# Kernel optimization log

Measured on AMD Instinct MI355X. Metric: run time of the kernel, lower is better.

The kernel has to match this reference:

```python
import jax, jax.numpy as jnp
import numpy as np

EMBED_DIM = 2048
HEAD_DIM = 128
BLOCK = 2048
BATCH = 8


def setup_inputs() -> dict:
    key = jax.random.key(0)
    kx, kq, kk, kv = jax.random.split(key, 4)
    x = jax.random.normal(kx, (BATCH, BLOCK, EMBED_DIM), dtype=jnp.float32)
    # torch nn.Linear(embed_dim, head_dim, bias=False) weight shape: [head_dim, embed_dim]
    s = 1.0 / np.sqrt(EMBED_DIM)
    Wq = jax.random.uniform(kq, (HEAD_DIM, EMBED_DIM), jnp.float32, -s, s)
    Wk = jax.random.uniform(kk, (HEAD_DIM, EMBED_DIM), jnp.float32, -s, s)
    Wv = jax.random.uniform(kv, (HEAD_DIM, EMBED_DIM), jnp.float32, -s, s)
    return {"x": x, "Wq": Wq, "Wk": Wk, "Wv": Wv}


def reference(x, Wq, Wk, Wv):
    B, T, C = x.shape
    # projections: y = x @ W.T
    q = jnp.einsum('btc,hc->bth', x, Wq)   # [B,T,H]
    k = jnp.einsum('btc,hc->bth', x, Wk)
    v = jnp.einsum('btc,hc->bth', x, Wv)
    # NOTE: original scales by embed_dim**0.5, not head_dim**0.5
    scale = 1.0 / jnp.sqrt(jnp.float32(C))
    logits = jnp.einsum('bth,bsh->bts', q, k) * scale  # [B,T,T]
    # causal mask (is_decoder=True)
    causal = jnp.tril(jnp.ones((T, T), dtype=bool))
    logits = jnp.where(causal, logits, -jnp.inf)
    weights = jax.nn.softmax(logits, axis=-1)
    attention = jnp.einsum('bts,bsh->bth', weights, v)  # [B,T,H]
    return attention
```

## Files before the change

kernel.cpp:

```cpp
#include <hip/hip_runtime.h>
#include <hip/hip_bf16.h>
#include <stdint.h>

constexpr int B    = 8;
constexpr int T    = 2048;
constexpr int EMB  = 2048;
constexpr int HD   = 128;
constexpr int M    = B * T;
constexpr int NW   = 3 * HD;

typedef __attribute__((ext_vector_type(8))) short short8;
typedef __attribute__((ext_vector_type(4))) float f32x4;

__device__ inline unsigned short f2bf(float f) {
    union { float f; unsigned int u; } v; v.f = f;
    unsigned int x = v.u;
    unsigned int r = (x + 0x7FFFu + ((x >> 16) & 1u)) >> 16;
    return (unsigned short)r;
}

__device__ inline unsigned int cvt_pk_bf16(float a, float b) {
    unsigned int r;
    asm volatile("v_cvt_pk_bf16_f32 %0, %1, %2" : "=v"(r) : "v"(a), "v"(b));
    return r;
}

__global__ __launch_bounds__(256) void conv_w(
    const float* __restrict__ Wq, const float* __restrict__ Wk, const float* __restrict__ Wv,
    unsigned short* __restrict__ Wb)
{
    int base = (blockIdx.x * 256 + threadIdx.x) * 8;
    int row = base >> 11, col = base & 2047;
    const float* src;
    if (row < 128)      src = Wq + (size_t)row * EMB + col;
    else if (row < 256) src = Wk + (size_t)(row - 128) * EMB + col;
    else                src = Wv + (size_t)(row - 256) * EMB + col;
    float4 a = *(const float4*)src;
    float4 b = *(const float4*)(src + 4);
    short8 sv;
    sv[0] = f2bf(a.x); sv[1] = f2bf(a.y); sv[2] = f2bf(a.z); sv[3] = f2bf(a.w);
    sv[4] = f2bf(b.x); sv[5] = f2bf(b.y); sv[6] = f2bf(b.z); sv[7] = f2bf(b.w);
    *(short8*)(Wb + base) = sv;
}

constexpr int PBM = 64;
constexpr int PBK = 64;
constexpr int PNT = EMB / PBK;

__global__ __launch_bounds__(512) void qkv_proj(
    const float* __restrict__ x, const unsigned short* __restrict__ Wb,
    unsigned short* __restrict__ Qb, unsigned short* __restrict__ Kb,
    unsigned short* __restrict__ VtG)
{
    __shared__ unsigned short Ab[2][PBM * PBK];
    __shared__ unsigned short Bb[2][NW * PBK];

    const int m0   = blockIdx.x * PBM;
    const int tid  = threadIdx.x;
    const int lane = tid & 63;
    const int w    = tid >> 6;
    const int lo   = lane & 15;
    const int hi   = lane >> 4;

    const int ar = tid >> 3;
    const int as = tid & 7;
    const float* asrc = x + (size_t)(m0 + ar) * EMB + as * 8;

    f32x4 acc[4][3];
#pragma unroll
    for (int i = 0; i < 4; ++i)
#pragma unroll
        for (int j = 0; j < 3; ++j) acc[i][j] = (f32x4)0.0f;

    short8 breg[6];
    float4 a0, a1;

    auto loadTile = [&](int k0) {
#pragma unroll
        for (int it = 0; it < 6; ++it) {
            int c = it * 512 + tid;
            int row = c >> 3, seg = c & 7;
            breg[it] = *(const short8*)(Wb + (size_t)row * EMB + k0 + seg * 8);
        }
        a0 = *(const float4*)(asrc + k0);
        a1 = *(const float4*)(asrc + k0 + 4);
    };
    auto writeTile = [&](int buf) {
#pragma unroll
        for (int it = 0; it < 6; ++it) {
            int c = it * 512 + tid;
            int row = c >> 3, seg = c & 7;
            *(short8*)&Bb[buf][row * PBK + ((seg ^ (row & 7))) * 8] = breg[it];
        }
        uint4 p;
        p.x = cvt_pk_bf16(a0.x, a0.y);
        p.y = cvt_pk_bf16(a0.z, a0.w);
        p.z = cvt_pk_bf16(a1.x, a1.y);
        p.w = cvt_pk_bf16(a1.z, a1.w);
        *(uint4*)&Ab[buf][ar * PBK + (as ^ (ar & 7)) * 8] = p;
    };
    auto compute = [&](int buf) {
#pragma unroll
        for (int kk = 0; kk < 2; ++kk) {
            short8 af[4], bf[3];
            const int cseg = kk * 4 + hi;
#pragma unroll
            for (int i = 0; i < 4; ++i) {
                int R = i * 16 + lo;
                af[i] = *(const short8*)&Ab[buf][R * PBK + (cseg ^ (R & 7)) * 8];
            }
#pragma unroll
            for (int j = 0; j < 3; ++j) {
                int n = w * 48 + j * 16 + lo;
                bf[j] = *(const short8*)&Bb[buf][n * PBK + (cseg ^ (n & 7)) * 8];
            }
#pragma unroll
            for (int i = 0; i < 4; ++i)
#pragma unroll
                for (int j = 0; j < 3; ++j)
                    acc[i][j] = __builtin_amdgcn_mfma_f32_16x16x32_bf16(af[i], bf[j], acc[i][j], 0, 0, 0);
        }
    };

    loadTile(0);
    writeTile(0);
    __syncthreads();

#pragma unroll 1
    for (int t = 0; t < PNT; ++t) {
        const int buf = t & 1;
        if (t + 1 < PNT) {
            loadTile((t + 1) * PBK);
            __builtin_amdgcn_sched_barrier(0);
        }
        compute(buf);
        if (t + 1 < PNT) {
            __builtin_amdgcn_sched_barrier(0);
            writeTile(buf ^ 1);
            __syncthreads();
        }
    }

    const int b = m0 >> 11;
#pragma unroll
    for (int i = 0; i < 4; ++i) {
        int mrow0 = m0 + i * 16 + hi * 4;
#pragma unroll
        for (int j = 0; j < 3; ++j) {
            int cw = w * 3 + j;
            int colbase = cw * 16 + lo;
            if (cw < 8) {
#pragma unroll
                for (int r = 0; r < 4; ++r)
                    Qb[(size_t)(mrow0 + r) * HD + colbase] = f2bf(acc[i][j][r]);
            } else if (cw < 16) {
#pragma unroll
                for (int r = 0; r < 4; ++r)
                    Kb[(size_t)(mrow0 + r) * HD + (colbase - 128)] = f2bf(acc[i][j][r]);
            } else {
                int h = colbase - 256;
                int tloc = mrow0 - b * T;
                ushort4 pv;
                pv.x = f2bf(acc[i][j][0]); pv.y = f2bf(acc[i][j][1]);
                pv.z = f2bf(acc[i][j][2]); pv.w = f2bf(acc[i][j][3]);
                *(ushort4*)(VtG + ((size_t)(b * HD + h)) * T + tloc) = pv;
            }
        }
    }
}

constexpr int QB = 64;
constexpr int KB = 64;
constexpr int STILES = 8;

__global__ __launch_bounds__(256) void attn_fwd(
    const unsigned short* __restrict__ Qb,
    const unsigned short* __restrict__ Kb,
    const unsigned short* __restrict__ VtG,
    float* __restrict__ out,
    float* __restrict__ part_o, float* __restrict__ part_ml,
    int use_split)
{
    const int b  = blockIdx.y;
    int bx = blockIdx.x;
    int qt, s, nsplit;
    if (use_split) {
        if (bx < 8)       { qt = bx;               s = 0; }
        else if (bx < 24) { qt = 8  + (bx - 8) / 2;  s = (bx - 8) & 1; }
        else if (bx < 48) { qt = 16 + (bx - 24) / 3; s = (bx - 24) % 3; }
        else              { qt = 24 + (bx - 48) / 4; s = (bx - 48) & 3; }
        nsplit = qt / 8 + 1;
    } else {
        qt = bx; s = 0; nsplit = 1;
    }
    const int q0 = qt * QB;
    int t0 = s * STILES;
    int t1 = t0 + STILES; if (t1 > qt + 1) t1 = qt + 1;

    const int tid  = threadIdx.x;
    const int lane = tid & 63;
    const int w    = tid >> 6;
    const int lo   = lane & 15;
    const int hi   = lane >> 4;

    __shared__ unsigned short Ks[KB][HD + 8];
    __shared__ unsigned short Vt[HD][KB + 16];
    __shared__ unsigned short Ps[QB][KB + 8];

    short8 qf[4];
    {
        int row = q0 + w * 16 + lo;
        const unsigned short* qp = Qb + ((size_t)b * T + row) * HD + hi * 8;
#pragma unroll
        for (int ks = 0; ks < 4; ++ks) qf[ks] = *(const short8*)(qp + ks * 32);
    }

    float mrow[4], lrow[4];
    f32x4 o[8];
#pragma unroll
    for (int r = 0; r < 4; ++r) { mrow[r] = -1e30f; lrow[r] = 0.0f; }
#pragma unroll
    for (int n = 0; n < 8; ++n) o[n] = (f32x4)0.0f;

    const float scale2 = 0.022097086912079608f * 1.4426950408889634f;
    const int qrow_base = q0 + w * 16 + hi * 4;

    for (int t = t0; t < t1; ++t) {
        const int kv0 = t * KB;
#pragma unroll
        for (int it = 0; it < 4; ++it) {
            int c = tid + it * 256;
            int row = c >> 4, c8 = (c & 15) * 8;
            *(short8*)&Ks[row][c8] =
                *(const short8*)(Kb + ((size_t)b * T + kv0 + row) * HD + c8);
        }
#pragma unroll
        for (int it = 0; it < 4; ++it) {
            int c = tid + it * 256;
            int row = c >> 3, c8 = (c & 7) * 8;
            *(short8*)&Vt[row][c8] =
                *(const short8*)(VtG + (size_t)(b * HD + row) * T + kv0 + c8);
        }
        __syncthreads();

        f32x4 sa[4];
#pragma unroll
        for (int j = 0; j < 4; ++j) sa[j] = (f32x4)0.0f;
#pragma unroll
        for (int ks = 0; ks < 4; ++ks) {
#pragma unroll
            for (int j = 0; j < 4; ++j) {
                short8 bf = *(const short8*)&Ks[j * 16 + lo][ks * 32 + hi * 8];
                sa[j] = __builtin_amdgcn_mfma_f32_16x16x32_bf16(qf[ks], bf, sa[j], 0, 0, 0);
            }
        }

        const bool diag = (t == qt);
        float alpha[4];
#pragma unroll
        for (int r = 0; r < 4; ++r) {
            const int qrow = qrow_base + r;
            float rm = -1e30f;
#pragma unroll
            for (int j = 0; j < 4; ++j) {
                float v = sa[j][r] * scale2;
                if (diag) {
                    int kv = kv0 + j * 16 + lo;
                    v = (kv <= qrow) ? v : -1e30f;
                }
                sa[j][r] = v;
                rm = fmaxf(rm, v);
            }
            rm = fmaxf(rm, __shfl_xor(rm, 1));
            rm = fmaxf(rm, __shfl_xor(rm, 2));
            rm = fmaxf(rm, __shfl_xor(rm, 4));
            rm = fmaxf(rm, __shfl_xor(rm, 8));
            float mn = fmaxf(mrow[r], rm);
            alpha[r] = exp2f(mrow[r] - mn);
            mrow[r] = mn;
            float ls = 0.0f;
#pragma unroll
            for (int j = 0; j < 4; ++j) {
                float p = exp2f(sa[j][r] - mn);
                sa[j][r] = p;
                ls += p;
            }
            ls += __shfl_xor(ls, 1);
            ls += __shfl_xor(ls, 2);
            ls += __shfl_xor(ls, 4);
            ls += __shfl_xor(ls, 8);
            lrow[r] = lrow[r] * alpha[r] + ls;
        }
#pragma unroll
        for (int n = 0; n < 8; ++n)
#pragma unroll
            for (int r = 0; r < 4; ++r) o[n][r] *= alpha[r];

#pragma unroll
        for (int r = 0; r < 4; ++r)
#pragma unroll
            for (int j = 0; j < 4; ++j)
                Ps[w * 16 + hi * 4 + r][j * 16 + lo] = f2bf(sa[j][r]);
        __syncthreads();

#pragma unroll
        for (int ks = 0; ks < 2; ++ks) {
            short8 af = *(const short8*)&Ps[w * 16 + lo][ks * 32 + hi * 8];
#pragma unroll
            for (int n = 0; n < 8; ++n) {
                short8 bv = *(const short8*)&Vt[n * 16 + lo][ks * 32 + hi * 8];
                o[n] = __builtin_amdgcn_mfma_f32_16x16x32_bf16(af, bv, o[n], 0, 0, 0);
            }
        }
        __syncthreads();
    }

    if (nsplit == 1) {
#pragma unroll
        for (int n = 0; n < 8; ++n) {
            int h = n * 16 + lo;
#pragma unroll
            for (int r = 0; r < 4; ++r) {
                int row = qrow_base + r;
                out[((size_t)b * T + row) * HD + h] = o[n][r] / lrow[r];
            }
        }
    } else {
        const size_t slot = (size_t)(b * 32 + qt) * 4 + s;
        float* po = part_o + slot * (QB * HD);
#pragma unroll
        for (int n = 0; n < 8; ++n) {
            int h = n * 16 + lo;
#pragma unroll
            for (int r = 0; r < 4; ++r)
                po[(w * 16 + hi * 4 + r) * HD + h] = o[n][r];
        }
        if (lo == 0) {
            float* pm = part_ml + slot * (QB * 2);
#pragma unroll
            for (int r = 0; r < 4; ++r) {
                pm[(w * 16 + hi * 4 + r) * 2 + 0] = mrow[r];
                pm[(w * 16 + hi * 4 + r) * 2 + 1] = lrow[r];
            }
        }
    }
}

__global__ __launch_bounds__(256) void attn_combine(
    const float* __restrict__ part_o, const float* __restrict__ part_ml,
    float* __restrict__ out)
{
    const int qt = 8 + blockIdx.x;
    const int b  = blockIdx.y;
    const int ns = qt / 8 + 1;
    const int tid = threadIdx.x;
    const int row = tid >> 2;
    const int c0  = (tid & 3) * 32;
    const size_t slot0 = (size_t)(b * 32 + qt) * 4;

    float mi[4], li[4];
    float m = -1e30f;
#pragma unroll 4
    for (int i = 0; i < ns; ++i) {
        mi[i] = part_ml[(slot0 + i) * (QB * 2) + row * 2 + 0];
        li[i] = part_ml[(slot0 + i) * (QB * 2) + row * 2 + 1];
        m = fmaxf(m, mi[i]);
    }
    float L = 0.0f, f[4];
#pragma unroll 4
    for (int i = 0; i < ns; ++i) {
        f[i] = exp2f(mi[i] - m);
        L += li[i] * f[i];
    }
    const float inv = 1.0f / L;

    float4 acc[8];
#pragma unroll
    for (int k = 0; k < 8; ++k) acc[k] = make_float4(0.f, 0.f, 0.f, 0.f);
#pragma unroll 4
    for (int i = 0; i < ns; ++i) {
        const float4* src = (const float4*)(part_o + (slot0 + i) * (QB * HD) + row * HD + c0);
#pragma unroll
        for (int k = 0; k < 8; ++k) {
            float4 v = src[k];
            acc[k].x += f[i] * v.x; acc[k].y += f[i] * v.y;
            acc[k].z += f[i] * v.z; acc[k].w += f[i] * v.w;
        }
    }
    float4* dst = (float4*)(out + ((size_t)b * T + qt * QB + row) * HD + c0);
#pragma unroll
    for (int k = 0; k < 8; ++k) {
        float4 v = acc[k];
        dst[k] = make_float4(v.x * inv, v.y * inv, v.z * inv, v.w * inv);
    }
}

extern "C" void kernel_launch(void* const* d_in, const int* in_sizes, int n_in,
                              void* d_out, int out_size, void* d_ws, size_t ws_size,
                              hipStream_t stream)
{
    const float* x  = (const float*)d_in[0];
    const float* Wq = (const float*)d_in[1];
    const float* Wk = (const float*)d_in[2];
    const float* Wv = (const float*)d_in[3];
    float* out = (float*)d_out;

    const size_t off_Wb = 0;
    const size_t off_Q  = off_Wb + (size_t)NW * EMB * 2;
    const size_t off_K  = off_Q  + (size_t)M * HD * 2;
    const size_t off_V  = off_K  + (size_t)M * HD * 2;
    const size_t off_po = off_V  + (size_t)M * HD * 2;
    const size_t off_ml = off_po + (size_t)1024 * QB * HD * 4;
    const size_t total  = off_ml + (size_t)1024 * QB * 2 * 4;

    char* ws = (char*)d_ws;
    unsigned short* Wb  = (unsigned short*)(ws + off_Wb);
    unsigned short* Qb  = (unsigned short*)(ws + off_Q);
    unsigned short* Kb  = (unsigned short*)(ws + off_K);
    unsigned short* VtG = (unsigned short*)(ws + off_V);
    float* part_o  = (float*)(ws + off_po);
    float* part_ml = (float*)(ws + off_ml);

    const int use_split = (ws_size >= total) ? 1 : 0;

    conv_w<<<dim3((NW * EMB) / (256 * 8)), 256, 0, stream>>>(Wq, Wk, Wv, Wb);
    qkv_proj<<<dim3(M / PBM), 512, 0, stream>>>(x, Wb, Qb, Kb, VtG);
    attn_fwd<<<dim3(use_split ? 80 : 32, B), 256, 0, stream>>>(
        Qb, Kb, VtG, out, part_o, part_ml, use_split);
    if (use_split)
        attn_combine<<<dim3(24, B), 256, 0, stream>>>(part_o, part_ml, out);
}
```

Baseline: 102.6 us.

## Split QKV projection over N into two 192-column tiles with XCD-aware block mapping

```diff
diff --git a/kernel.cpp b/kernel.cpp
--- a/kernel.cpp
+++ b/kernel.cpp
@@ -44,27 +44,35 @@
 }
 
 constexpr int PBM = 64;
+constexpr int PBN = 192;
 constexpr int PBK = 64;
 constexpr int PNT = EMB / PBK;
 
-__global__ __launch_bounds__(512) void qkv_proj(
+__global__ __launch_bounds__(256, 2) void qkv_proj(
     const float* __restrict__ x, const unsigned short* __restrict__ Wb,
     unsigned short* __restrict__ Qb, unsigned short* __restrict__ Kb,
     unsigned short* __restrict__ VtG)
 {
     __shared__ unsigned short Ab[2][PBM * PBK];
-    __shared__ unsigned short Bb[2][NW * PBK];
-
-    const int m0   = blockIdx.x * PBM;
+    __shared__ unsigned short Bb[2][PBN * PBK];
+
+    const int d   = blockIdx.x;
+    const int xcd = d & 7;
+    const int g   = d >> 3;
+    const int mt  = xcd * 32 + (g >> 1);
+    const int ns  = g & 1;
+    const int m0  = mt * PBM;
+    const int n0  = ns * PBN;
+
     const int tid  = threadIdx.x;
     const int lane = tid & 63;
     const int w    = tid >> 6;
     const int lo   = lane & 15;
     const int hi   = lane >> 4;
 
-    const int ar = tid >> 3;
-    const int as = tid & 7;
-    const float* asrc = x + (size_t)(m0 + ar) * EMB + as * 8;
+    const int ar = tid >> 2;
+    const int s0 = (tid & 3) * 2;
+    const float* asrc = x + (size_t)(m0 + ar) * EMB + s0 * 8;
 
     f32x4 acc[4][3];
 #pragma unroll
@@ -73,31 +81,34 @@
         for (int j = 0; j < 3; ++j) acc[i][j] = (f32x4)0.0f;
 
     short8 breg[6];
-    float4 a0, a1;
+    float4 a0, a1, a2, a3;
 
     auto loadTile = [&](int k0) {
 #pragma unroll
         for (int it = 0; it < 6; ++it) {
-            int c = it * 512 + tid;
+            int c = it * 256 + tid;
             int row = c >> 3, seg = c & 7;
-            breg[it] = *(const short8*)(Wb + (size_t)row * EMB + k0 + seg * 8);
+            breg[it] = *(const short8*)(Wb + (size_t)(n0 + row) * EMB + k0 + seg * 8);
         }
         a0 = *(const float4*)(asrc + k0);
         a1 = *(const float4*)(asrc + k0 + 4);
+        a2 = *(const float4*)(asrc + k0 + 8);
+        a3 = *(const float4*)(asrc + k0 + 12);
     };
     auto writeTile = [&](int buf) {
 #pragma unroll
         for (int it = 0; it < 6; ++it) {
-            int c = it * 512 + tid;
+            int c = it * 256 + tid;
             int row = c >> 3, seg = c & 7;
-            *(short8*)&Bb[buf][row * PBK + ((seg ^ (row & 7))) * 8] = breg[it];
-        }
-        uint4 p;
-        p.x = cvt_pk_bf16(a0.x, a0.y);
-        p.y = cvt_pk_bf16(a0.z, a0.w);
-        p.z = cvt_pk_bf16(a1.x, a1.y);
-        p.w = cvt_pk_bf16(a1.z, a1.w);
-        *(uint4*)&Ab[buf][ar * PBK + (as ^ (ar & 7)) * 8] = p;
+            *(short8*)&Bb[buf][row * PBK + (seg ^ (row & 7)) * 8] = breg[it];
+        }
+        uint4 p0, p1;
+        p0.x = cvt_pk_bf16(a0.x, a0.y);  p0.y = cvt_pk_bf16(a0.z, a0.w);
+        p0.z = cvt_pk_bf16(a1.x, a1.y);  p0.w = cvt_pk_bf16(a1.z, a1.w);
+        p1.x = cvt_pk_bf16(a2.x, a2.y);  p1.y = cvt_pk_bf16(a2.z, a2.w);
+        p1.z = cvt_pk_bf16(a3.x, a3.y);  p1.w = cvt_pk_bf16(a3.z, a3.w);
+        *(uint4*)&Ab[buf][ar * PBK + ((s0    ) ^ (ar & 7)) * 8] = p0;
+        *(uint4*)&Ab[buf][ar * PBK + ((s0 + 1) ^ (ar & 7)) * 8] = p1;
     };
     auto compute = [&](int buf) {
 #pragma unroll
@@ -147,13 +158,12 @@
         int mrow0 = m0 + i * 16 + hi * 4;
 #pragma unroll
         for (int j = 0; j < 3; ++j) {
-            int cw = w * 3 + j;
-            int colbase = cw * 16 + lo;
-            if (cw < 8) {
+            int colbase = n0 + w * 48 + j * 16 + lo;
+            if (colbase < 128) {
 #pragma unroll
                 for (int r = 0; r < 4; ++r)
                     Qb[(size_t)(mrow0 + r) * HD + colbase] = f2bf(acc[i][j][r]);
-            } else if (cw < 16) {
+            } else if (colbase < 256) {
 #pragma unroll
                 for (int r = 0; r < 4; ++r)
                     Kb[(size_t)(mrow0 + r) * HD + (colbase - 128)] = f2bf(acc[i][j][r]);
@@ -424,7 +434,7 @@
     const int use_split = (ws_size >= total) ? 1 : 0;
 
     conv_w<<<dim3((NW * EMB) / (256 * 8)), 256, 0, stream>>>(Wq, Wk, Wv, Wb);
-    qkv_proj<<<dim3(M / PBM), 512, 0, stream>>>(x, Wb, Qb, Kb, VtG);
+    qkv_proj<<<dim3(512), 256, 0, stream>>>(x, Wb, Qb, Kb, VtG);
     attn_fwd<<<dim3(use_split ? 80 : 32, B), 256, 0, stream>>>(
         Qb, Kb, VtG, out, part_o, part_ml, use_split);
     if (use_split)
```

After: 101.3 us. About the same (-1.3%).
